# Kernel optimization log

Hardware: AMD Instinct MI355X
Metric: run time of the kernel (lower is better)

Reference implementation:

```python
import jax, jax.numpy as jnp
import numpy as np

D = 256
B, S, N = 4, 512, 4


def setup_inputs() -> dict:
    key = jax.random.key(0)
    ks = jax.random.split(key, 24)
    d, dq = D, D // 4
    std = 0.02
    inp = {
        'x':   jax.random.normal(ks[0], (B, S, N, d), jnp.float32),
        'Wq':  jax.random.normal(ks[1], (d, d), jnp.float32) * std,
        'Wk':  jax.random.normal(ks[2], (d, d), jnp.float32) * std,
        'Wv':  jax.random.normal(ks[3], (d, d), jnp.float32) * std,
        'Wg1': jax.random.normal(ks[4], (d, d), jnp.float32) * std,
        'bg1': jnp.zeros((d,), jnp.float32),
        'Wg2': jax.random.normal(ks[5], (d, d), jnp.float32) * std,
        'bg2': jnp.zeros((d,), jnp.float32),
        'We1': jax.random.normal(ks[6], (d, dq), jnp.float32) * std,
        'be1': jnp.zeros((dq,), jnp.float32),
        'We2': jax.random.normal(ks[7], (dq, 1), jnp.float32) * std,
        'be2': jnp.zeros((1,), jnp.float32),
        'Wa1': jax.random.normal(ks[8], (d, dq), jnp.float32) * std,
        'ba1': jnp.zeros((dq,), jnp.float32),
        'Wa2': jax.random.normal(ks[9], (dq, 1), jnp.float32) * std,
        'ba2': jnp.zeros((1,), jnp.float32),
        'Wo':  jax.random.normal(ks[10], (d, d), jnp.float32) * std,
        'bo':  jnp.zeros((d,), jnp.float32),
        'gamma': jnp.ones((d,), jnp.float32),
        'beta':  jnp.zeros((d,), jnp.float32),
    }
    return inp


def reference(x, Wq, Wk, Wv, Wg1, bg1, Wg2, bg2, We1, be1, We2, be2,
              Wa1, ba1, Wa2, ba2, Wo, bo, gamma, beta):
    b, s, n, f = x.shape
    xf = x.reshape(b * n, s, f)  # matches torch .view on contiguous x
    residual = xf

    q = xf @ Wq                                    # [bn, s, d]
    k = xf @ Wk
    v = xf @ Wv
    v_hat = jax.nn.silu(v @ Wg1 + bg1) @ Wg2 + bg2  # value_generator
    eta = jax.nn.sigmoid(jax.nn.silu(xf @ We1 + be1) @ We2 + be2) * 0.1 + 0.01   # [bn, s, 1]
    alpha = jax.nn.sigmoid(jax.nn.silu(xf @ Wa1 + ba1) @ Wa2 + ba2) * 0.5 + 0.5  # [bn, s, 1]

    # F.normalize(k, dim=-1): eps = 1e-12
    kn = k / jnp.maximum(jnp.linalg.norm(k, axis=-1, keepdims=True), 1e-12)

    M0 = jnp.zeros((b * n, f, f), x.dtype)

    def step(M, inp):
        q_t, k_t, v_t, e_t, a_t = inp  # [bn,d],[bn,d],[bn,d],[bn,1],[bn,1]
        out_t = jnp.einsum('bij,bj->bi', M, q_t)
        Mk = jnp.einsum('bij,bj->bi', M, k_t)
        e = e_t[:, :, None]  # [bn,1,1]
        a = a_t[:, :, None]
        # delta rule: M <- a*M - e*(Mk k^T) + e*(v k^T)
        M_new = a * M + e * ((v_t - Mk)[:, :, None] * k_t[:, None, :])
        return M_new, out_t

    seq = (jnp.swapaxes(q, 0, 1), jnp.swapaxes(kn, 0, 1), jnp.swapaxes(v_hat, 0, 1),
           jnp.swapaxes(eta, 0, 1), jnp.swapaxes(alpha, 0, 1))
    M, outs = jax.lax.scan(step, M0, seq)
    out = jnp.swapaxes(outs, 0, 1)  # [bn, s, d]

    y = out @ Wo + bo + residual  # dropout is identity in eval/reference
    mu = jnp.mean(y, axis=-1, keepdims=True)
    var = jnp.var(y, axis=-1, keepdims=True)
    y = (y - mu) / jnp.sqrt(var + 1e-5) * gamma + beta
    return y.reshape(b, s, n, f), M
```

## Files before the change

kernel.cpp:

```cpp
#include <hip/hip_runtime.h>

#define F_ 256
#define S_ 512
#define NH_ 16
#define CCH 32
#define NCH (S_/CCH)
#define KSTR 264
#define KTSTR 36
#define TSTR 40

typedef __attribute__((ext_vector_type(8))) short short8_t;
typedef __attribute__((ext_vector_type(4))) float f32x4;

__device__ __forceinline__ float sigmoid_f(float x) { return 1.0f / (1.0f + __expf(-x)); }

__device__ __forceinline__ ushort f2bf(float x) {
  uint u = __float_as_uint(x);
  u += 0x7FFFu + ((u >> 16) & 1u);
  return (ushort)(u >> 16);
}
__device__ __forceinline__ float bf2f(ushort u) {
  return __uint_as_float((uint)u << 16);
}

template<int CTRL>
__device__ __forceinline__ float dpp_add(float x) {
  int y = __builtin_amdgcn_update_dpp(0, __float_as_int(x), CTRL, 0xf, 0xf, true);
  return x + __int_as_float(y);
}
__device__ __forceinline__ float red8(float x) {
  x = dpp_add<0xB1>(x);
  x = dpp_add<0x4E>(x);
  x = dpp_add<0x141>(x);
  return x;
}

__global__ __launch_bounds__(256) void wconv_k(
    const float* __restrict__ Wq, const float* __restrict__ Wk,
    const float* __restrict__ Wv, const float* __restrict__ Wg1,
    const float* __restrict__ Wg2, const float* __restrict__ Wo,
    const float* __restrict__ We1, const float* __restrict__ Wa1,
    const float* __restrict__ be1, const float* __restrict__ ba1,
    ushort* __restrict__ Wt, float* __restrict__ beas)
{
  const int blk = blockIdx.x, tid = threadIdx.x;
  if (blk == 104) {
    if (tid < 64) beas[tid] = be1[tid];
    else if (tid < 128) beas[tid] = ba1[tid - 64];
    return;
  }
  __shared__ float tile[64][65];
  const float* src; int N, k0, n0; size_t dstbase;
  if (blk < 96) {
    const int w = blk >> 4, tl = blk & 15;
    const float* ws_[6] = {Wq, Wk, Wv, Wg1, Wg2, Wo};
    const size_t dstb[6] = {0, 65536, 131072, 229376, 294912, 360448};
    src = ws_[w]; N = 256;
    k0 = (tl >> 2) * 64; n0 = (tl & 3) * 64;
    dstbase = dstb[w];
  } else {
    const int w = (blk - 96) >> 2, tl = (blk - 96) & 3;
    src = w ? Wa1 : We1; N = 64;
    k0 = tl * 64; n0 = 0;
    dstbase = w ? 212992 : 196608;
  }
// ... 131 lines not shown
    pB[0] = *(const short8_t*)&Wt[(size_t)(col0 + r_) * 256 + k0 + c8_];
    pB[1] = *(const short8_t*)&Wt[(size_t)(col0 + 32 + r_) * 256 + k0 + c8_];
  };
  auto commitT = [&](int b) {
    *(short8_t*)&As[b][r_ * 72 + c8_] = pA[0];
    *(short8_t*)&As[b][(32 + r_) * 72 + c8_] = pA[1];
    *(short8_t*)&Ws[b][r_ * 72 + c8_] = pB[0];
    *(short8_t*)&Ws[b][(32 + r_) * 72 + c8_] = pB[1];
  };

  f32x4 acc[2][2];
  #pragma unroll
  for (int i = 0; i < 2; ++i)
    #pragma unroll
    for (int j = 0; j < 2; ++j)
      #pragma unroll
      for (int r = 0; r < 4; ++r) acc[i][j][r] = 0.f;

  loadT(0); commitT(0); __syncthreads();
  #pragma unroll
  for (int t = 0; t < 4; ++t) {
    const int b = t & 1;
    if (t < 3) loadT((t + 1) << 6);
    #pragma unroll
    for (int kk = 0; kk < 2; ++kk) {
      short8_t a0 = *(const short8_t*)&As[b][(wr * 32 + ln) * 72 + kk * 32 + hi8];
      short8_t a1 = *(const short8_t*)&As[b][(wr * 32 + 16 + ln) * 72 + kk * 32 + hi8];
      short8_t b0 = *(const short8_t*)&Ws[b][(wc * 32 + ln) * 72 + kk * 32 + hi8];
      short8_t b1 = *(const short8_t*)&Ws[b][(wc * 32 + 16 + ln) * 72 + kk * 32 + hi8];
      acc[0][0] = __builtin_amdgcn_mfma_f32_16x16x32_bf16(a0, b0, acc[0][0], 0, 0, 0);
      acc[0][1] = __builtin_amdgcn_mfma_f32_16x16x32_bf16(a0, b1, acc[0][1], 0, 0, 0);
      acc[1][0] = __builtin_amdgcn_mfma_f32_16x16x32_bf16(a1, b0, acc[1][0], 0, 0, 0);
      acc[1][1] = __builtin_amdgcn_mfma_f32_16x16x32_bf16(a1, b1, acc[1][1], 0, 0, 0);
    }
    if (t < 3) commitT(b ^ 1);
    __syncthreads();
  }

  #pragma unroll
  for (int mi = 0; mi < 2; ++mi)
    #pragma unroll
    for (int ni = 0; ni < 2; ++ni) {
      const int col = col0 + wc * 32 + ni * 16 + ln;
      const float bval = bias ? bias[col] : 0.f;
      #pragma unroll
      for (int r = 0; r < 4; ++r) {
        const int row = row0 + wr * 32 + mi * 16 + hi4 + r;
        float vx = acc[mi][ni][r] + bval;
        if (act == 1) vx = vx * sigmoid_f(vx);
        if (Cf) Cf[(size_t)row * 256 + col] = vx;
        if (Cb) Cb[(size_t)row * 256 + col] = f2bf(vx);
      }
    }
}

__global__ __launch_bounds__(256) void gemmo_ln_k(
    const ushort* __restrict__ A, const ushort* __restrict__ Wt,
    const float* __restrict__ bo, const float* __restrict__ x,
    const float* __restrict__ gamma, const float* __restrict__ beta,
    float* __restrict__ y)
{
  __shared__ ushort As[2][32 * 72];
  __shared__ ushort Ws[2][256 * 72];
  __shared__ float rs_[2][32];
  __shared__ float rq_[2][32];
  const int tid = threadIdx.x;
  const int wv = tid >> 6, l = tid & 63;
  const int ln = l & 15, hi = l >> 4, hi4 = hi << 2, hi8 = hi << 3;
  const int g = wv >> 1, chf = wv & 1;
  const int row0 = blockIdx.x * 32;

  short8_t pA, pW[8];
  auto loadT = [&](int k0) {
    { const int r = tid >> 3, c8 = (tid & 7) << 3;
      pA = *(const short8_t*)&A[(size_t)(row0 + r) * 256 + k0 + c8]; }
    #pragma unroll
    for (int p = 0; p < 8; ++p) {
      const int idx = (p << 8) + tid;
      const int n = idx >> 3, c8 = (idx & 7) << 3;
      pW[p] = *(const short8_t*)&Wt[(size_t)n * 256 + k0 + c8];
    }
  };
  auto commitT = [&](int b) {
    { const int r = tid >> 3, c8 = (tid & 7) << 3;
      *(short8_t*)&As[b][r * 72 + c8] = pA; }
    #pragma unroll
    for (int p = 0; p < 8; ++p) {
      const int idx = (p << 8) + tid;
      const int n = idx >> 3, c8 = (idx & 7) << 3;
      *(short8_t*)&Ws[b][n * 72 + c8] = pW[p];
    }
  };

  f32x4 acc[8];
  #pragma unroll
  for (int nt = 0; nt < 8; ++nt)
    #pragma unroll
    for (int r = 0; r < 4; ++r) acc[nt][r] = 0.f;

  loadT(0); commitT(0); __syncthreads();
  #pragma unroll
  for (int t = 0; t < 4; ++t) {
    const int b = t & 1;
    if (t < 3) loadT((t + 1) << 6);
    #pragma unroll
    for (int kk = 0; kk < 2; ++kk) {
// ... 42 lines not shown
  #pragma unroll
  for (int r = 0; r < 4; ++r) {
    const int lr = g * 16 + hi4 + r;
    const float tot = rs_[0][lr] + rs_[1][lr];
    const float tq  = rq_[0][lr] + rq_[1][lr];
    const float mu  = tot * (1.0f / 256.0f);
    const float var = tq * (1.0f / 256.0f) - mu * mu;
    const float rstd = rsqrtf(var + 1e-5f);
    #pragma unroll
    for (int nt = 0; nt < 8; ++nt) {
      const int col = chf * 128 + nt * 16 + ln;
      y[(size_t)(row0 + lr) * 256 + col] =
          (val[nt][r] - mu) * rstd * gamma[col] + beta[col];
    }
  }
}

__global__ __launch_bounds__(256) void knea_k(
    const float* __restrict__ kf, ushort* __restrict__ kb,
    const float* __restrict__ sesa,
    const float* __restrict__ We2, const float* __restrict__ be2,
    const float* __restrict__ Wa2, const float* __restrict__ ba2,
    float* __restrict__ eta, float* __restrict__ alpha)
{
  const int lane = threadIdx.x & 63;
  const size_t row = ((size_t)blockIdx.x << 2) + (threadIdx.x >> 6);
  {
    const size_t off = row * F_ + ((size_t)lane << 2);
    float4 v = *(const float4*)&kf[off];
    float ss = v.x * v.x + v.y * v.y + v.z * v.z + v.w * v.w;
    #pragma unroll
    for (int m = 1; m < 64; m <<= 1) ss += __shfl_xor(ss, m, 64);
    const float sc = 1.0f / fmaxf(sqrtf(ss), 1e-12f);
    ushort4 o;
    o.x = f2bf(v.x * sc); o.y = f2bf(v.y * sc);
    o.z = f2bf(v.z * sc); o.w = f2bf(v.w * sc);
    *(ushort4*)&kb[off] = o;
  }
  {
    float pe = sesa[row * 128 + lane] * We2[lane];
    float pa = sesa[row * 128 + 64 + lane] * Wa2[lane];
    #pragma unroll
    for (int m = 1; m < 64; m <<= 1) {
      pe += __shfl_xor(pe, m, 64);
      pa += __shfl_xor(pa, m, 64);
    }
    if (lane == 0) {
      eta[row]   = sigmoid_f(pe + be2[0]) * 0.1f + 0.01f;
      alpha[row] = sigmoid_f(pa + ba2[0]) * 0.5f + 0.5f;
    }
  }
}

__global__ __launch_bounds__(256) void prep_k(
    const ushort* __restrict__ kb, const ushort* __restrict__ qb,
    const float* __restrict__ eta, const float* __restrict__ alpha,
    ushort* __restrict__ Tg, ushort* __restrict__ Gqg, float* __restrict__ Sg,
    ushort* __restrict__ Ktg)
{
  __shared__ ushort K_lds[CCH * KSTR];
  __shared__ ushort Q_lds[CCH * KSTR];
  __shared__ float  G_lds[CCH * CCH];
  __shared__ float  ea[2 * CCH];
  __shared__ float  scal[100];

  const int tid = threadIdx.x;
  const int ch = blockIdx.x, h = blockIdx.y;
  const int t0 = ch * CCH;
  const int l = tid & 63, wv = tid >> 6;
  const int ln = l & 15, hi = l >> 4;
  const int hi8 = hi * 8, hi4 = hi * 4;

  const ushort* kg = kb + (size_t)(h * S_ + t0) * F_;
  const ushort* qg = qb + (size_t)(h * S_ + t0) * F_;
  #pragma unroll
  for (int w = 0; w < 4; ++w) {
    int o = w * 256 + tid; int t = o >> 5, c8 = (o & 31) << 3;
    *(short8_t*)&K_lds[t * KSTR + c8] = *(const short8_t*)&kg[(size_t)t * F_ + c8];
    *(short8_t*)&Q_lds[t * KSTR + c8] = *(const short8_t*)&qg[(size_t)t * F_ + c8];
  }
  if (tid < CCH)            ea[tid] = eta[(size_t)h * S_ + t0 + tid];
  else if (tid < 2 * CCH)   ea[tid] = alpha[(size_t)h * S_ + t0 + tid - CCH];
  __syncthreads();

  {
    const int tt = tid & 31, cl = tid >> 5;
    for (int cp = 0; cp < 32; ++cp) {
      const int c = cp * 8 + cl;
      Ktg[((size_t)h * F_ + c) * S_ + t0 + tt] = K_lds[tt * KSTR + c];
    }
  }

  {
    const int tI = wv >> 1, tJ = wv & 1;
    f32x4 accG = {0.f, 0.f, 0.f, 0.f};
    f32x4 accQ = {0.f, 0.f, 0.f, 0.f};
    #pragma unroll
    for (int ko = 0; ko < 8; ++ko) {
      const int cb = ko * 32 + hi8;
      short8_t bfr = *(const short8_t*)&K_lds[(tJ * 16 + ln) * KSTR + cb];
      short8_t aK  = *(const short8_t*)&K_lds[(tI * 16 + ln) * KSTR + cb];
      short8_t aQ  = *(const short8_t*)&Q_lds[(tI * 16 + ln) * KSTR + cb];
      accG = __builtin_amdgcn_mfma_f32_16x16x32_bf16(aK, bfr, accG, 0, 0, 0);
      accQ = __builtin_amdgcn_mfma_f32_16x16x32_bf16(aQ, bfr, accQ, 0, 0, 0);
    }
    ushort* Gqo = Gqg + (size_t)(h * NCH + ch) * (CCH * CCH);
    #pragma unroll
    for (int r = 0; r < 4; ++r) {
      const int t = tI * 16 + hi4 + r, s = tJ * 16 + ln;
      G_lds[t * CCH + s] = accG[r];
      Gqo[t * CCH + s] = (s < t) ? f2bf(accQ[r]) : (ushort)0;
    }
  }
  if (tid == 0) {
    float gp = 1.f;
    for (int t = 0; t < CCH; ++t) {
      const float a = ea[CCH + t], e = ea[t];
      const float gm = gp * a;
      scal[t]           = e / a;
      scal[CCH + t]     = e / gm;
      scal[2 * CCH + t] = gp;
      gp = gm;
    }
    scal[3 * CCH] = gp;
  }
  __syncthreads();

  {
    const int j = tid >> 3, g = tid & 7;
    float x0 = 0.f, x1 = 0.f, x2 = 0.f, x3 = 0.f;
    ushort* To = Tg + (size_t)(h * NCH + ch) * (CCH * CCH);
    #pragma unroll
    for (int t = 0; t < CCH; ++t) {
      float p = 0.f;
      const f32x4 gr = *(const f32x4*)&G_lds[t * CCH + 4 * g];
      if (4 * g + 0 < t) p += gr[0] * x0;
      if (4 * g + 1 < t) p += gr[1] * x1;
      if (4 * g + 2 < t) p += gr[2] * x2;
      if (4 * g + 3 < t) p += gr[3] * x3;
      const float tot = red8(p);
      const float xt = ((t == j) ? 1.f : 0.f) - scal[t] * tot;
      if (g == (t >> 2)) {
        if ((t & 3) == 0) x0 = xt; else if ((t & 3) == 1) x1 = xt;
        else if ((t & 3) == 2) x2 = xt; else x3 = xt;
      }
      if (g == 0) To[t * CCH + j] = f2bf(xt);
    }
  }
  if (tid < 97) Sg[(size_t)(h * NCH + ch) * 128 + tid] = scal[tid];
}

__global__ __launch_bounds__(256, 1) void scan_chunk_k(
    const ushort* __restrict__ kb, const ushort* __restrict__ qb,
    const ushort* __restrict__ vhb, const ushort* __restrict__ Ktg,
    const ushort* __restrict__ Tg, const ushort* __restrict__ Gqg,
    const float* __restrict__ Sg,
    ushort* __restrict__ outb, float* __restrict__ Mout)
{
  __shared__ ushort K_lds[2][CCH * KSTR];
  __shared__ ushort Q_lds[2][CCH * KSTR];
  __shared__ ushort Kt_lds[2][F_ * KTSTR];
  __shared__ ushort M_lds[16 * KSTR];
  __shared__ ushort T_lds[2][CCH * TSTR];
  __shared__ ushort Gq_lds[2][CCH * TSTR];
  __shared__ ushort Wt_lds[16 * TSTR];
  __shared__ ushort R_lds[16 * TSTR];
  __shared__ float  QM_lds[CCH * 20];
  __shared__ ushort V_lds[2][CCH * 16];
  __shared__ float  scal[2][104];

  const int tid = threadIdx.x;
  const int flat = blockIdx.x;
  const int h = (flat & 7) + (((flat >> 3) >> 4) << 3);
  const int slice = (flat >> 3) & 15;
  const int r0 = slice * 16;
  const int wv = tid >> 6, l = tid & 63;
  const int ln = l & 15, hi = l >> 4, hi4 = hi << 2, hi8 = hi << 3;

  for (int u = tid; u < 16 * KSTR / 8; u += 256) {
    short8_t z = {0, 0, 0, 0, 0, 0, 0, 0};
    *(short8_t*)&M_lds[u * 8] = z;
  }
  f32x4 Mf[4];
  #pragma unroll
  for (int q = 0; q < 4; ++q)
    #pragma unroll
    for (int r = 0; r < 4; ++r) Mf[q][r] = 0.f;

  const ushort* kgh = kb + (size_t)h * S_ * F_;
  const ushort* qgh = qb + (size_t)h * S_ * F_;
  const ushort* kth = Ktg + (size_t)h * F_ * S_;

  short8_t pK[4], pQ[4], pKt[4], pTG;
  ushort pV[2]; float pS = 0.f;

  auto loadchunk = [&](int ch) {
    const int t0 = ch * CCH;
    #pragma unroll
    for (int r = 0; r < 4; ++r) {
      const int idx = (r << 8) + tid;
      const int t = idx >> 5, c8 = (idx & 31) << 3;
      pK[r] = *(const short8_t*)&kgh[(size_t)(t0 + t) * F_ + c8];
      pQ[r] = *(const short8_t*)&qgh[(size_t)(t0 + t) * F_ + c8];
    }
    #pragma unroll
    for (int r = 0; r < 4; ++r) {
      const int idx = (r << 8) + tid;
      const int c = idx >> 2, t8 = (idx & 3) << 3;
      pKt[r] = *(const short8_t*)&kth[(size_t)c * S_ + t0 + t8];
    }
    #pragma unroll
    for (int u = 0; u < 2; ++u) {
      const int e = (u << 8) + tid, t = e >> 4, i = e & 15;
      pV[u] = vhb[(size_t)(h * S_ + t0 + t) * F_ + r0 + i];
    }
    {
      const ushort* Ti = Tg  + (size_t)(h * NCH + ch) * (CCH * CCH);
      const ushort* Gi = Gqg + (size_t)(h * NCH + ch) * (CCH * CCH);
      if (tid < 128) {
        const int t = tid >> 2, c8 = (tid & 3) << 3;
        pTG = *(const short8_t*)&Ti[t * CCH + c8];
      } else {
        const int t = (tid - 128) >> 2, c8 = ((tid - 128) & 3) << 3;
        pTG = *(const short8_t*)&Gi[t * CCH + c8];
      }
    }
    if (tid < 97) pS = Sg[(size_t)(h * NCH + ch) * 128 + tid];
  };

  auto commit = [&](int buf) {
    #pragma unroll
    for (int r = 0; r < 4; ++r) {
      const int idx = (r << 8) + tid;
      const int t = idx >> 5, c8 = (idx & 31) << 3;
      *(short8_t*)&K_lds[buf][t * KSTR + c8] = pK[r];
      *(short8_t*)&Q_lds[buf][t * KSTR + c8] = pQ[r];
    }
    #pragma unroll
    for (int r = 0; r < 4; ++r) {
      const int idx = (r << 8) + tid;
      const int c = idx >> 2, t8 = (idx & 3) << 3;
      *(short8_t*)&Kt_lds[buf][c * KTSTR + t8] = pKt[r];
    }
    #pragma unroll
    for (int u = 0; u < 2; ++u) V_lds[buf][(u << 8) + tid] = pV[u];
    if (tid < 128) {
      const int t = tid >> 2, c8 = (tid & 3) << 3;
      *(short8_t*)&T_lds[buf][t * TSTR + c8] = pTG;
    } else {
      const int t = (tid - 128) >> 2, c8 = ((tid - 128) & 3) << 3;
      *(short8_t*)&Gq_lds[buf][t * TSTR + c8] = pTG;
    }
    if (tid < 97) scal[buf][tid] = pS;
  };

  loadchunk(0);
  commit(0);
  __syncthreads();

  for (int ch = 0; ch < NCH; ++ch) {
    const int buf = ch & 1;
    const int t0 = ch * CCH;
    if (ch + 1 < NCH) loadchunk(ch + 1);

    if (wv < 2) {
      const int I = wv;
      f32x4 a0 = {0.f, 0.f, 0.f, 0.f}, a1 = {0.f, 0.f, 0.f, 0.f};
      #pragma unroll
      for (int ko = 0; ko < 4; ++ko) {
        {
          short8_t a = *(const short8_t*)&K_lds[buf][(I * 16 + ln) * KSTR + (2 * ko) * 32 + hi8];
          short8_t b = *(const short8_t*)&M_lds[ln * KSTR + (2 * ko) * 32 + hi8];
          a0 = __builtin_amdgcn_mfma_f32_16x16x32_bf16(a, b, a0, 0, 0, 0);
        }
        {
          short8_t a = *(const short8_t*)&K_lds[buf][(I * 16 + ln) * KSTR + (2 * ko + 1) * 32 + hi8];
          short8_t b = *(const short8_t*)&M_lds[ln * KSTR + (2 * ko + 1) * 32 + hi8];
          a1 = __builtin_amdgcn_mfma_f32_16x16x32_bf16(a, b, a1, 0, 0, 0);
        }
      }
      #pragma unroll
      for (int r = 0; r < 4; ++r) {
        const int t = I * 16 + hi4 + r;
        const float s = a0[r] + a1[r];
        const float rhs = scal[buf][CCH + t] * bf2f(V_lds[buf][t * 16 + ln])
                        - scal[buf][t] * s;
        R_lds[ln * TSTR + t] = f2bf(rhs);
      }
    } else {
      const int I = wv - 2;
      f32x4 a0 = {0.f, 0.f, 0.f, 0.f}, a1 = {0.f, 0.f, 0.f, 0.f};
      #pragma unroll
      for (int ko = 0; ko < 4; ++ko) {
        {
          short8_t a = *(const short8_t*)&Q_lds[buf][(I * 16 + ln) * KSTR + (2 * ko) * 32 + hi8];
          short8_t b = *(const short8_t*)&M_lds[ln * KSTR + (2 * ko) * 32 + hi8];
          a0 = __builtin_amdgcn_mfma_f32_16x16x32_bf16(a, b, a0, 0, 0, 0);
        }
        {
          short8_t a = *(const short8_t*)&Q_lds[buf][(I * 16 + ln) * KSTR + (2 * ko + 1) * 32 + hi8];
          short8_t b = *(const short8_t*)&M_lds[ln * KSTR + (2 * ko + 1) * 32 + hi8];
          a1 = __builtin_amdgcn_mfma_f32_16x16x32_bf16(a, b, a1, 0, 0, 0);
        }
      }
      #pragma unroll
      for (int r = 0; r < 4; ++r)
        QM_lds[(I * 16 + hi4 + r) * 20 + ln] = a0[r] + a1[r];
    }
    __syncthreads();

    if (wv < 2) {
      const int I = wv;
      short8_t a = *(const short8_t*)&T_lds[buf][(I * 16 + ln) * TSTR + hi8];
      short8_t b = *(const short8_t*)&R_lds[ln * TSTR + hi8];
      f32x4 z = {0.f, 0.f, 0.f, 0.f};
      f32x4 d = __builtin_amdgcn_mfma_f32_16x16x32_bf16(a, b, z, 0, 0, 0);
      #pragma unroll
      for (int r = 0; r < 4; ++r)
        Wt_lds[ln * TSTR + I * 16 + hi4 + r] = f2bf(d[r]);
    }
    __syncthreads();

    if (wv < 2) {
      const int I = wv;
      short8_t a = *(const short8_t*)&Gq_lds[buf][(I * 16 + ln) * TSTR + hi8];
      short8_t b = *(const short8_t*)&Wt_lds[ln * TSTR + hi8];
      f32x4 z = {0.f, 0.f, 0.f, 0.f};
      f32x4 d = __builtin_amdgcn_mfma_f32_16x16x32_bf16(a, b, z, 0, 0, 0);
      #pragma unroll
      for (int r = 0; r < 4; ++r) {
        const int t = I * 16 + hi4 + r;
        outb[(size_t)(h * S_ + t0 + t) * F_ + r0 + ln] =
            f2bf(scal[buf][2 * CCH + t] * (QM_lds[t * 20 + ln] + d[r]));
      }
    }
    {
      const float gC = scal[buf][3 * CCH];
      short8_t aw = *(const short8_t*)&Wt_lds[ln * TSTR + hi8];
      #pragma unroll
      for (int qq = 0; qq < 4; ++qq) {
        const int jt = wv * 4 + qq;
        short8_t bk = *(const short8_t*)&Kt_lds[buf][(jt * 16 + ln) * KTSTR + hi8];
        f32x4 d = __builtin_amdgcn_mfma_f32_16x16x32_bf16(aw, bk, Mf[qq], 0, 0, 0);
        #pragma unroll
        for (int r = 0; r < 4; ++r) {
          const float nv = gC * d[r];
          Mf[qq][r] = nv;
          M_lds[(hi4 + r) * KSTR + jt * 16 + ln] = f2bf(nv);
        }
      }
    }
    if (ch + 1 < NCH) commit(buf ^ 1);
    __syncthreads();
  }

  #pragma unroll
  for (int qq = 0; qq < 4; ++qq) {
    const int jt = wv * 4 + qq;
    #pragma unroll
    for (int r = 0; r < 4; ++r)
      Mout[((size_t)h * F_ + r0 + hi4 + r) * F_ + jt * 16 + ln] = Mf[qq][r];
  }
}

extern "C" void kernel_launch(void* const* d_in, const int* in_sizes, int n_in,
                              void* d_out, int out_size, void* d_ws, size_t ws_size,
                              hipStream_t stream)
{
  const float* x    = (const float*)d_in[0];
  const float* Wq   = (const float*)d_in[1];
  const float* Wk   = (const float*)d_in[2];
  const float* Wv   = (const float*)d_in[3];
  const float* Wg1  = (const float*)d_in[4];
  const float* bg1  = (const float*)d_in[5];
  const float* Wg2  = (const float*)d_in[6];
  const float* bg2  = (const float*)d_in[7];
  const float* We1  = (const float*)d_in[8];
  const float* be1  = (const float*)d_in[9];
  const float* We2  = (const float*)d_in[10];
  const float* be2  = (const float*)d_in[11];
  const float* Wa1  = (const float*)d_in[12];
  const float* ba1  = (const float*)d_in[13];
  const float* Wa2  = (const float*)d_in[14];
  const float* ba2  = (const float*)d_in[15];
  const float* Wo   = (const float*)d_in[16];
  const float* bo   = (const float*)d_in[17];
  const float* gamma= (const float*)d_in[18];
  const float* beta = (const float*)d_in[19];

  const int Mrows = NH_ * S_;
  const size_t MM = 1048576;
  const size_t NTF = 2 * MM;

  float* ws = (float*)d_ws;
  ushort* outb = (ushort*)(ws + 0 * MM);
  ushort* qb   = (ushort*)(ws + 1 * MM);
  ushort* kb   = (ushort*)(ws + 2 * MM);
  float*  kf   = ws + 3 * MM;
  ushort* t1b  = (ushort*)(ws + 3 * MM);
  ushort* vhb  = (ushort*)(ws + 4 * MM);
  ushort* vb   = (ushort*)(ws + 5 * MM);
  float*  sesa = ws + 6 * MM;
  float*  eta  = ws + 7 * MM;
  float*  alpha= eta + Mrows;
  ushort* Tg   = (ushort*)(ws + 7 * MM + 16384);
  ushort* Gqg  = Tg + 262144;
  float*  Sg   = ws + 7 * MM + 16384 + 131072 + 131072;
  ushort* Ktg  = (ushort*)(Sg + 32768);
  ushort* Wt   = Ktg + 2097152;
  float*  beas = (float*)(Wt + 425984);

  dim3 blk(256);

  wconv_k<<<105, blk, 0, stream>>>(Wq, Wk, Wv, Wg1, Wg2, Wo, We1, Wa1,
                                   be1, ba1, Wt, beas);

  qkve_k<<<dim3(14, 128), blk, 0, stream>>>(x, Wt, beas, qb, kf, vb, sesa);

  knea_k<<<Mrows / 4, blk, 0, stream>>>(kf, kb, sesa, We2, be2, Wa2, ba2, eta, alpha);

  gemm_bf16_k<<<dim3(4, 128), blk, 0, stream>>>(vb,  Wt + 229376, bg1, nullptr, t1b, 1);
  gemm_bf16_k<<<dim3(4, 128), blk, 0, stream>>>(t1b, Wt + 294912, bg2, nullptr, vhb, 0);

  prep_k<<<dim3(NCH, NH_), blk, 0, stream>>>(kb, qb, eta, alpha, Tg, Gqg, Sg, Ktg);

  float* yout = (float*)d_out;
  float* Mfin = yout + NTF;
  scan_chunk_k<<<256, blk, 0, stream>>>(kb, qb, vhb, Ktg, Tg, Gqg, Sg, outb, Mfin);

  gemmo_ln_k<<<256, blk, 0, stream>>>(outb, Wt + 360448, bo, x, gamma, beta, yout);
}
```

Measured before the change: 100.1 us.

## Split scan into 8-row slices with single-buffered LDS and two blocks per CU

The chunked delta-rule scan now gives each block 8 rows of the state instead of 16, so 512 blocks launch instead of 256. Double-buffered LDS tiles become single buffers with the commit split into two phases, which cuts shared memory so two blocks fit per CU under the new launch bounds. The output-projection MFMA is moved after the state update. Each block still runs full 16-wide MFMAs with half the lanes masked off, so compute per useful row doubles in exchange for more parallelism and occupancy.

```diff
diff --git a/kernel.cpp b/kernel.cpp
--- a/kernel.cpp
+++ b/kernel.cpp
@@ -494,30 +494,31 @@
   if (tid < 97) Sg[(size_t)(h * NCH + ch) * 128 + tid] = scal[tid];
 }
 
-__global__ __launch_bounds__(256, 1) void scan_chunk_k(
+__global__ __launch_bounds__(256, 2) void scan_chunk_k(
     const ushort* __restrict__ kb, const ushort* __restrict__ qb,
     const ushort* __restrict__ vhb, const ushort* __restrict__ Ktg,
     const ushort* __restrict__ Tg, const ushort* __restrict__ Gqg,
     const float* __restrict__ Sg,
     ushort* __restrict__ outb, float* __restrict__ Mout)
 {
-  __shared__ ushort K_lds[2][CCH * KSTR];
-  __shared__ ushort Q_lds[2][CCH * KSTR];
-  __shared__ ushort Kt_lds[2][F_ * KTSTR];
+  __shared__ ushort K_lds[CCH * KSTR];
+  __shared__ ushort Q_lds[CCH * KSTR];
+  __shared__ ushort Kt_lds[F_ * KTSTR];
   __shared__ ushort M_lds[16 * KSTR];
-  __shared__ ushort T_lds[2][CCH * TSTR];
-  __shared__ ushort Gq_lds[2][CCH * TSTR];
+  __shared__ ushort T_lds[CCH * TSTR];
+  __shared__ ushort Gq_lds[CCH * TSTR];
   __shared__ ushort Wt_lds[16 * TSTR];
   __shared__ ushort R_lds[16 * TSTR];
-  __shared__ float  QM_lds[CCH * 20];
-  __shared__ ushort V_lds[2][CCH * 16];
+  __shared__ float  QM_lds[CCH * 12];
+  __shared__ ushort V_lds[CCH * 8];
   __shared__ float  scal[2][104];
 
   const int tid = threadIdx.x;
   const int flat = blockIdx.x;
-  const int h = (flat & 7) + (((flat >> 3) >> 4) << 3);
-  const int slice = (flat >> 3) & 15;
-  const int r0 = slice * 16;
+  const int idx = flat >> 3;
+  const int h = (flat & 7) + ((idx >> 5) << 3);
+  const int slice = idx & 31;
+  const int r0 = slice * 8;
   const int wv = tid >> 6, l = tid & 63;
   const int ln = l & 15, hi = l >> 4, hi4 = hi << 2, hi8 = hi << 3;
 
@@ -534,30 +535,27 @@
   const ushort* kgh = kb + (size_t)h * S_ * F_;
   const ushort* qgh = qb + (size_t)h * S_ * F_;
   const ushort* kth = Ktg + (size_t)h * F_ * S_;
+  const ushort* vgh = vhb + (size_t)h * S_ * F_;
 
   short8_t pK[4], pQ[4], pKt[4], pTG;
-  ushort pV[2]; float pS = 0.f;
+  ushort pV = 0; float pS = 0.f;
 
   auto loadchunk = [&](int ch) {
     const int t0 = ch * CCH;
     #pragma unroll
     for (int r = 0; r < 4; ++r) {
-      const int idx = (r << 8) + tid;
-      const int t = idx >> 5, c8 = (idx & 31) << 3;
+      const int idx2 = (r << 8) + tid;
+      const int t = idx2 >> 5, c8 = (idx2 & 31) << 3;
       pK[r] = *(const short8_t*)&kgh[(size_t)(t0 + t) * F_ + c8];
       pQ[r] = *(const short8_t*)&qgh[(size_t)(t0 + t) * F_ + c8];
     }
     #pragma unroll
     for (int r = 0; r < 4; ++r) {
-      const int idx = (r << 8) + tid;
-      const int c = idx >> 2, t8 = (idx & 3) << 3;
+      const int idx2 = (r << 8) + tid;
+      const int c = idx2 >> 2, t8 = (idx2 & 3) << 3;
       pKt[r] = *(const short8_t*)&kth[(size_t)c * S_ + t0 + t8];
     }
-    #pragma unroll
-    for (int u = 0; u < 2; ++u) {
-      const int e = (u << 8) + tid, t = e >> 4, i = e & 15;
-      pV[u] = vhb[(size_t)(h * S_ + t0 + t) * F_ + r0 + i];
-    }
+    pV = vgh[(size_t)(t0 + (tid >> 3)) * F_ + r0 + (tid & 7)];
     {
       const ushort* Ti = Tg  + (size_t)(h * NCH + ch) * (CCH * CCH);
       const ushort* Gi = Gqg + (size_t)(h * NCH + ch) * (CCH * CCH);
@@ -572,39 +570,43 @@
     if (tid < 97) pS = Sg[(size_t)(h * NCH + ch) * 128 + tid];
   };
 
-  auto commit = [&](int buf) {
+  auto commitA = [&](int dst) {
     #pragma unroll
     for (int r = 0; r < 4; ++r) {
-      const int idx = (r << 8) + tid;
-      const int t = idx >> 5, c8 = (idx & 31) << 3;
-      *(short8_t*)&K_lds[buf][t * KSTR + c8] = pK[r];
-      *(short8_t*)&Q_lds[buf][t * KSTR + c8] = pQ[r];
-    }
-    #pragma unroll
-    for (int r = 0; r < 4; ++r) {
-      const int idx = (r << 8) + tid;
-      const int c = idx >> 2, t8 = (idx & 3) << 3;
-      *(short8_t*)&Kt_lds[buf][c * KTSTR + t8] = pKt[r];
-    }
-    #pragma unroll
-    for (int u = 0; u < 2; ++u) V_lds[buf][(u << 8) + tid] = pV[u];
+      const int idx2 = (r << 8) + tid;
+      const int t = idx2 >> 5, c8 = (idx2 & 31) << 3;
+      *(short8_t*)&K_lds[t * KSTR + c8] = pK[r];
+      *(short8_t*)&Q_lds[t * KSTR + c8] = pQ[r];
+    }
+    V_lds[tid] = pV;
     if (tid < 128) {
       const int t = tid >> 2, c8 = (tid & 3) << 3;
-      *(short8_t*)&T_lds[buf][t * TSTR + c8] = pTG;
-    } else {
+      *(short8_t*)&T_lds[t * TSTR + c8] = pTG;
+    }
+    if (tid < 97) scal[dst][tid] = pS;
+  };
+  auto commitB = [&]() {
+    #pragma unroll
+    for (int r = 0; r < 4; ++r) {
+      const int idx2 = (r << 8) + tid;
+      const int c = idx2 >> 2, t8 = (idx2 & 3) << 3;
+      *(short8_t*)&Kt_lds[c * KTSTR + t8] = pKt[r];
+    }
+    if (tid >= 128) {
       const int t = (tid - 128) >> 2, c8 = ((tid - 128) & 3) << 3;
-      *(short8_t*)&Gq_lds[buf][t * TSTR + c8] = pTG;
-    }
-    if (tid < 97) scal[buf][tid] = pS;
+      *(short8_t*)&Gq_lds[t * TSTR + c8] = pTG;
+    }
   };
 
   loadchunk(0);
-  commit(0);
+  commitA(0);
+  commitB();
   __syncthreads();
 
   for (int ch = 0; ch < NCH; ++ch) {
-    const int buf = ch & 1;
+    const int sb = ch & 1;
     const int t0 = ch * CCH;
+    if (ch > 0) commitB();
     if (ch + 1 < NCH) loadchunk(ch + 1);
 
     if (wv < 2) {
@@ -613,12 +615,12 @@
       #pragma unroll
       for (int ko = 0; ko < 4; ++ko) {
         {
-          short8_t a = *(const short8_t*)&K_lds[buf][(I * 16 + ln) * KSTR + (2 * ko) * 32 + hi8];
+          short8_t a = *(const short8_t*)&K_lds[(I * 16 + ln) * KSTR + (2 * ko) * 32 + hi8];
           short8_t b = *(const short8_t*)&M_lds[ln * KSTR + (2 * ko) * 32 + hi8];
           a0 = __builtin_amdgcn_mfma_f32_16x16x32_bf16(a, b, a0, 0, 0, 0);
         }
         {
-          short8_t a = *(const short8_t*)&K_lds[buf][(I * 16 + ln) * KSTR + (2 * ko + 1) * 32 + hi8];
+          short8_t a = *(const short8_t*)&K_lds[(I * 16 + ln) * KSTR + (2 * ko + 1) * 32 + hi8];
           short8_t b = *(const short8_t*)&M_lds[ln * KSTR + (2 * ko + 1) * 32 + hi8];
           a1 = __builtin_amdgcn_mfma_f32_16x16x32_bf16(a, b, a1, 0, 0, 0);
         }
@@ -626,10 +628,14 @@
       #pragma unroll
       for (int r = 0; r < 4; ++r) {
         const int t = I * 16 + hi4 + r;
-        const float s = a0[r] + a1[r];
-        const float rhs = scal[buf][CCH + t] * bf2f(V_lds[buf][t * 16 + ln])
-                        - scal[buf][t] * s;
-        R_lds[ln * TSTR + t] = f2bf(rhs);
+        ushort rw = 0;
+        if (ln < 8) {
+          const float s = a0[r] + a1[r];
+          const float rhs = scal[sb][CCH + t] * bf2f(V_lds[t * 8 + ln])
+                          - scal[sb][t] * s;
+          rw = f2bf(rhs);
+        }
+        R_lds[ln * TSTR + t] = rw;
       }
     } else {
       const int I = wv - 2;
@@ -637,25 +643,27 @@
       #pragma unroll
       for (int ko = 0; ko < 4; ++ko) {
         {
-          short8_t a = *(const short8_t*)&Q_lds[buf][(I * 16 + ln) * KSTR + (2 * ko) * 32 + hi8];
+          short8_t a = *(const short8_t*)&Q_lds[(I * 16 + ln) * KSTR + (2 * ko) * 32 + hi8];
           short8_t b = *(const short8_t*)&M_lds[ln * KSTR + (2 * ko) * 32 + hi8];
           a0 = __builtin_amdgcn_mfma_f32_16x16x32_bf16(a, b, a0, 0, 0, 0);
         }
         {
-          short8_t a = *(const short8_t*)&Q_lds[buf][(I * 16 + ln) * KSTR + (2 * ko + 1) * 32 + hi8];
+          short8_t a = *(const short8_t*)&Q_lds[(I * 16 + ln) * KSTR + (2 * ko + 1) * 32 + hi8];
           short8_t b = *(const short8_t*)&M_lds[ln * KSTR + (2 * ko + 1) * 32 + hi8];
           a1 = __builtin_amdgcn_mfma_f32_16x16x32_bf16(a, b, a1, 0, 0, 0);
         }
       }
-      #pragma unroll
-      for (int r = 0; r < 4; ++r)
-        QM_lds[(I * 16 + hi4 + r) * 20 + ln] = a0[r] + a1[r];
+      if (ln < 8) {
+        #pragma unroll
+        for (int r = 0; r < 4; ++r)
+          QM_lds[(I * 16 + hi4 + r) * 12 + ln] = a0[r] + a1[r];
+      }
     }
     __syncthreads();
 
     if (wv < 2) {
       const int I = wv;
-      short8_t a = *(const short8_t*)&T_lds[buf][(I * 16 + ln) * TSTR + hi8];
+      short8_t a = *(const short8_t*)&T_lds[(I * 16 + ln) * TSTR + hi8];
       short8_t b = *(const short8_t*)&R_lds[ln * TSTR + hi8];
       f32x4 z = {0.f, 0.f, 0.f, 0.f};
       f32x4 d = __builtin_amdgcn_mfma_f32_16x16x32_bf16(a, b, z, 0, 0, 0);
@@ -665,26 +673,13 @@
     }
     __syncthreads();
 
-    if (wv < 2) {
-      const int I = wv;
-      short8_t a = *(const short8_t*)&Gq_lds[buf][(I * 16 + ln) * TSTR + hi8];
-      short8_t b = *(const short8_t*)&Wt_lds[ln * TSTR + hi8];
-      f32x4 z = {0.f, 0.f, 0.f, 0.f};
-      f32x4 d = __builtin_amdgcn_mfma_f32_16x16x32_bf16(a, b, z, 0, 0, 0);
-      #pragma unroll
-      for (int r = 0; r < 4; ++r) {
-        const int t = I * 16 + hi4 + r;
-        outb[(size_t)(h * S_ + t0 + t) * F_ + r0 + ln] =
-            f2bf(scal[buf][2 * CCH + t] * (QM_lds[t * 20 + ln] + d[r]));
-      }
-    }
     {
-      const float gC = scal[buf][3 * CCH];
+      const float gC = scal[sb][3 * CCH];
       short8_t aw = *(const short8_t*)&Wt_lds[ln * TSTR + hi8];
       #pragma unroll
       for (int qq = 0; qq < 4; ++qq) {
         const int jt = wv * 4 + qq;
-        short8_t bk = *(const short8_t*)&Kt_lds[buf][(jt * 16 + ln) * KTSTR + hi8];
+        short8_t bk = *(const short8_t*)&Kt_lds[(jt * 16 + ln) * KTSTR + hi8];
         f32x4 d = __builtin_amdgcn_mfma_f32_16x16x32_bf16(aw, bk, Mf[qq], 0, 0, 0);
         #pragma unroll
         for (int r = 0; r < 4; ++r) {
@@ -694,16 +689,33 @@
         }
       }
     }
-    if (ch + 1 < NCH) commit(buf ^ 1);
+    if (wv < 2) {
+      const int I = wv;
+      short8_t a = *(const short8_t*)&Gq_lds[(I * 16 + ln) * TSTR + hi8];
+      short8_t b = *(const short8_t*)&Wt_lds[ln * TSTR + hi8];
+      f32x4 z = {0.f, 0.f, 0.f, 0.f};
+      f32x4 d = __builtin_amdgcn_mfma_f32_16x16x32_bf16(a, b, z, 0, 0, 0);
+      if (ln < 8) {
+        #pragma unroll
+        for (int r = 0; r < 4; ++r) {
+          const int t = I * 16 + hi4 + r;
+          outb[(size_t)(h * S_ + t0 + t) * F_ + r0 + ln] =
+              f2bf(scal[sb][2 * CCH + t] * (QM_lds[t * 12 + ln] + d[r]));
+        }
+      }
+    }
+    if (ch + 1 < NCH) commitA(sb ^ 1);
     __syncthreads();
   }
 
-  #pragma unroll
-  for (int qq = 0; qq < 4; ++qq) {
-    const int jt = wv * 4 + qq;
-    #pragma unroll
-    for (int r = 0; r < 4; ++r)
-      Mout[((size_t)h * F_ + r0 + hi4 + r) * F_ + jt * 16 + ln] = Mf[qq][r];
+  if (hi < 2) {
+    #pragma unroll
+    for (int qq = 0; qq < 4; ++qq) {
+      const int jt = wv * 4 + qq;
+      #pragma unroll
+      for (int r = 0; r < 4; ++r)
+        Mout[((size_t)h * F_ + r0 + hi4 + r) * F_ + jt * 16 + ln] = Mf[qq][r];
+    }
   }
 }
 
@@ -770,7 +782,7 @@
 
   float* yout = (float*)d_out;
   float* Mfin = yout + NTF;
-  scan_chunk_k<<<256, blk, 0, stream>>>(kb, qb, vhb, Ktg, Tg, Gqg, Sg, outb, Mfin);
+  scan_chunk_k<<<512, blk, 0, stream>>>(kb, qb, vhb, Ktg, Tg, Gqg, Sg, outb, Mfin);
 
   gemmo_ln_k<<<256, blk, 0, stream>>>(outb, Wt + 360448, bo, x, gamma, beta, yout);
 }
```

Result: slower. 108.5 us (+8.3%).

## Merge first value-generator GEMM with chunk prep and trim scan barriers

Applied to the files above, without the earlier changes.

Combines the Wg1 GEMM and the per-chunk prep work into one launch, with blocks picking a role by block index. This removes a kernel launch and lets the two independent jobs fill the GPU at the same time. In the scan kernel, waves 0-1 each compute both halves of the residual and then their W tile privately, which removes two block-wide barriers per chunk. The output GEMM is moved after the M update, and the barriers are replaced by raw waitcnt+s_barrier. The tradeoff is duplicated K·M MFMA work in each of those two waves and a tighter reliance on LDS ordering.

```diff
diff --git a/kernel.cpp b/kernel.cpp
--- a/kernel.cpp
+++ b/kernel.cpp
@@ -11,6 +11,12 @@
 
 typedef __attribute__((ext_vector_type(8))) short short8_t;
 typedef __attribute__((ext_vector_type(4))) float f32x4;
+
+#define BARX() do { \
+  asm volatile("s_waitcnt lgkmcnt(0)" ::: "memory"); \
+  __builtin_amdgcn_s_barrier(); \
+  __builtin_amdgcn_sched_barrier(0); \
+} while (0)
 
 __device__ __forceinline__ float sigmoid_f(float x) { return 1.0f / (1.0f + __expf(-x)); }
 
@@ -248,6 +254,176 @@
         if (Cb) Cb[(size_t)row * 256 + col] = f2bf(vx);
       }
     }
+}
+
+__global__ __launch_bounds__(256) void g1prep_k(
+    const ushort* __restrict__ vb, const ushort* __restrict__ WtG1,
+    const float* __restrict__ bg1, ushort* __restrict__ t1b,
+    const ushort* __restrict__ kb, const ushort* __restrict__ qb,
+    const float* __restrict__ eta, const float* __restrict__ alpha,
+    ushort* __restrict__ Tg, ushort* __restrict__ Gqg, float* __restrict__ Sg,
+    ushort* __restrict__ Ktg)
+{
+  __shared__ __align__(16) char smem[38592];
+  const int blk = blockIdx.x;
+  const int tid = threadIdx.x;
+  const int l = tid & 63, wv = tid >> 6;
+  const int ln = l & 15, hi = l >> 4, hi4 = hi << 2, hi8 = hi << 3;
+
+  if (blk < 512) {
+    ushort* As = (ushort*)smem;
+    ushort* Ws = (ushort*)(smem + 18432);
+    const int wr = wv >> 1, wc = wv & 1;
+    const int row0 = (blk >> 2) * 64, col0 = (blk & 3) * 64;
+    const int r_ = tid >> 3, c8_ = (tid & 7) << 3;
+
+    short8_t pA[2], pB[2];
+    auto loadT = [&](int k0) {
+      pA[0] = *(const short8_t*)&vb[(size_t)(row0 + r_) * 256 + k0 + c8_];
+      pA[1] = *(const short8_t*)&vb[(size_t)(row0 + 32 + r_) * 256 + k0 + c8_];
+      pB[0] = *(const short8_t*)&WtG1[(size_t)(col0 + r_) * 256 + k0 + c8_];
+      pB[1] = *(const short8_t*)&WtG1[(size_t)(col0 + 32 + r_) * 256 + k0 + c8_];
+    };
+    auto commitT = [&](int b) {
+      *(short8_t*)&As[b * 4608 + r_ * 72 + c8_] = pA[0];
+      *(short8_t*)&As[b * 4608 + (32 + r_) * 72 + c8_] = pA[1];
+      *(short8_t*)&Ws[b * 4608 + r_ * 72 + c8_] = pB[0];
+      *(short8_t*)&Ws[b * 4608 + (32 + r_) * 72 + c8_] = pB[1];
+    };
+
+    f32x4 acc[2][2];
+    #pragma unroll
+    for (int i = 0; i < 2; ++i)
+      #pragma unroll
+      for (int j = 0; j < 2; ++j)
+        #pragma unroll
+        for (int r = 0; r < 4; ++r) acc[i][j][r] = 0.f;
+
+    loadT(0); commitT(0); __syncthreads();
+    #pragma unroll
+    for (int t = 0; t < 4; ++t) {
+      const int b = t & 1;
+      if (t < 3) loadT((t + 1) << 6);
+      #pragma unroll
+      for (int kk = 0; kk < 2; ++kk) {
+        short8_t a0 = *(const short8_t*)&As[b * 4608 + (wr * 32 + ln) * 72 + kk * 32 + hi8];
+        short8_t a1 = *(const short8_t*)&As[b * 4608 + (wr * 32 + 16 + ln) * 72 + kk * 32 + hi8];
+        short8_t b0 = *(const short8_t*)&Ws[b * 4608 + (wc * 32 + ln) * 72 + kk * 32 + hi8];
+        short8_t b1 = *(const short8_t*)&Ws[b * 4608 + (wc * 32 + 16 + ln) * 72 + kk * 32 + hi8];
+        acc[0][0] = __builtin_amdgcn_mfma_f32_16x16x32_bf16(a0, b0, acc[0][0], 0, 0, 0);
+        acc[0][1] = __builtin_amdgcn_mfma_f32_16x16x32_bf16(a0, b1, acc[0][1], 0, 0, 0);
+        acc[1][0] = __builtin_amdgcn_mfma_f32_16x16x32_bf16(a1, b0, acc[1][0], 0, 0, 0);
+        acc[1][1] = __builtin_amdgcn_mfma_f32_16x16x32_bf16(a1, b1, acc[1][1], 0, 0, 0);
+      }
+      if (t < 3) commitT(b ^ 1);
+      __syncthreads();
+    }
+
+    #pragma unroll
+    for (int mi = 0; mi < 2; ++mi)
+      #pragma unroll
+      for (int ni = 0; ni < 2; ++ni) {
+        const int col = col0 + wc * 32 + ni * 16 + ln;
+        const float bval = bg1[col];
+        #pragma unroll
+        for (int r = 0; r < 4; ++r) {
+          const int row = row0 + wr * 32 + mi * 16 + hi4 + r;
+          float vx = acc[mi][ni][r] + bval;
+          vx = vx * sigmoid_f(vx);
+          t1b[(size_t)row * 256 + col] = f2bf(vx);
+        }
+      }
+    return;
+  }
+
+  const int pb = blk - 512;
+  const int ch = pb & 15, h = pb >> 4;
+  const int t0 = ch * CCH;
+  ushort* K_lds = (ushort*)smem;
+  ushort* Q_lds = (ushort*)(smem + 16896);
+  float*  G_lds = (float*)(smem + 33792);
+  float*  ea    = (float*)(smem + 37888);
+  float*  eaA   = (float*)(smem + 37888 + 0);
+  float*  scal  = (float*)(smem + 38144);
+
+  const ushort* kg = kb + (size_t)(h * S_ + t0) * F_;
+  const ushort* qg = qb + (size_t)(h * S_ + t0) * F_;
+  #pragma unroll
+  for (int w = 0; w < 4; ++w) {
+    int o = w * 256 + tid; int t = o >> 5, c8 = (o & 31) << 3;
+    *(short8_t*)&K_lds[t * KSTR + c8] = *(const short8_t*)&kg[(size_t)t * F_ + c8];
+    *(short8_t*)&Q_lds[t * KSTR + c8] = *(const short8_t*)&qg[(size_t)t * F_ + c8];
+  }
+  if (tid < CCH)            ea[tid] = eta[(size_t)h * S_ + t0 + tid];
+  else if (tid < 2 * CCH)   ea[tid] = alpha[(size_t)h * S_ + t0 + tid - CCH];
+  __syncthreads();
+  (void)eaA;
+
+  {
+    const int tt = tid & 31, cl = tid >> 5;
+    for (int cp = 0; cp < 32; ++cp) {
+      const int c = cp * 8 + cl;
+      Ktg[((size_t)h * F_ + c) * S_ + t0 + tt] = K_lds[tt * KSTR + c];
+    }
+  }
+
+  {
+    const int tI = wv >> 1, tJ = wv & 1;
+    f32x4 accG = {0.f, 0.f, 0.f, 0.f};
+    f32x4 accQ = {0.f, 0.f, 0.f, 0.f};
+    #pragma unroll
+    for (int ko = 0; ko < 8; ++ko) {
+      const int cb = ko * 32 + hi8;
+      short8_t bfr = *(const short8_t*)&K_lds[(tJ * 16 + ln) * KSTR + cb];
+      short8_t aK  = *(const short8_t*)&K_lds[(tI * 16 + ln) * KSTR + cb];
+      short8_t aQ  = *(const short8_t*)&Q_lds[(tI * 16 + ln) * KSTR + cb];
+      accG = __builtin_amdgcn_mfma_f32_16x16x32_bf16(aK, bfr, accG, 0, 0, 0);
+      accQ = __builtin_amdgcn_mfma_f32_16x16x32_bf16(aQ, bfr, accQ, 0, 0, 0);
+    }
+    ushort* Gqo = Gqg + (size_t)(h * NCH + ch) * (CCH * CCH);
+    #pragma unroll
+    for (int r = 0; r < 4; ++r) {
+      const int t = tI * 16 + hi4 + r, s = tJ * 16 + ln;
+      G_lds[t * CCH + s] = accG[r];
+      Gqo[t * CCH + s] = (s < t) ? f2bf(accQ[r]) : (ushort)0;
+    }
+  }
+  if (tid == 0) {
+    float gp = 1.f;
+    for (int t = 0; t < CCH; ++t) {
+      const float a = ea[CCH + t], e = ea[t];
+      const float gm = gp * a;
+      scal[t]           = e / a;
+      scal[CCH + t]     = e / gm;
+      scal[2 * CCH + t] = gp;
+      gp = gm;
+    }
+    scal[3 * CCH] = gp;
+  }
+  __syncthreads();
+
+  {
+    const int j = tid >> 3, g = tid & 7;
+    float x0 = 0.f, x1 = 0.f, x2 = 0.f, x3 = 0.f;
+    ushort* To = Tg + (size_t)(h * NCH + ch) * (CCH * CCH);
+    #pragma unroll
+    for (int t = 0; t < CCH; ++t) {
+      float p = 0.f;
+      const f32x4 gr = *(const f32x4*)&G_lds[t * CCH + 4 * g];
+      if (4 * g + 0 < t) p += gr[0] * x0;
+      if (4 * g + 1 < t) p += gr[1] * x1;
+      if (4 * g + 2 < t) p += gr[2] * x2;
+      if (4 * g + 3 < t) p += gr[3] * x3;
+      const float tot = red8(p);
+      const float xt = ((t == j) ? 1.f : 0.f) - scal[t] * tot;
+      if (g == (t >> 2)) {
+        if ((t & 3) == 0) x0 = xt; else if ((t & 3) == 1) x1 = xt;
+        else if ((t & 3) == 2) x2 = xt; else x3 = xt;
+      }
+      if (g == 0) To[t * CCH + j] = f2bf(xt);
+    }
+  }
+  if (tid < 97) Sg[(size_t)(h * NCH + ch) * 128 + tid] = scal[tid];
 }
 
 __global__ __launch_bounds__(256) void gemmo_ln_k(
@@ -396,104 +572,6 @@
   }
 }
 
-__global__ __launch_bounds__(256) void prep_k(
-    const ushort* __restrict__ kb, const ushort* __restrict__ qb,
-    const float* __restrict__ eta, const float* __restrict__ alpha,
-    ushort* __restrict__ Tg, ushort* __restrict__ Gqg, float* __restrict__ Sg,
-    ushort* __restrict__ Ktg)
-{
-  __shared__ ushort K_lds[CCH * KSTR];
-  __shared__ ushort Q_lds[CCH * KSTR];
-  __shared__ float  G_lds[CCH * CCH];
-  __shared__ float  ea[2 * CCH];
-  __shared__ float  scal[100];
-
-  const int tid = threadIdx.x;
-  const int ch = blockIdx.x, h = blockIdx.y;
-  const int t0 = ch * CCH;
-  const int l = tid & 63, wv = tid >> 6;
-  const int ln = l & 15, hi = l >> 4;
-  const int hi8 = hi * 8, hi4 = hi * 4;
-
-  const ushort* kg = kb + (size_t)(h * S_ + t0) * F_;
-  const ushort* qg = qb + (size_t)(h * S_ + t0) * F_;
-  #pragma unroll
-  for (int w = 0; w < 4; ++w) {
-    int o = w * 256 + tid; int t = o >> 5, c8 = (o & 31) << 3;
-    *(short8_t*)&K_lds[t * KSTR + c8] = *(const short8_t*)&kg[(size_t)t * F_ + c8];
-    *(short8_t*)&Q_lds[t * KSTR + c8] = *(const short8_t*)&qg[(size_t)t * F_ + c8];
-  }
-  if (tid < CCH)            ea[tid] = eta[(size_t)h * S_ + t0 + tid];
-  else if (tid < 2 * CCH)   ea[tid] = alpha[(size_t)h * S_ + t0 + tid - CCH];
-  __syncthreads();
-
-  {
-    const int tt = tid & 31, cl = tid >> 5;
-    for (int cp = 0; cp < 32; ++cp) {
-      const int c = cp * 8 + cl;
-      Ktg[((size_t)h * F_ + c) * S_ + t0 + tt] = K_lds[tt * KSTR + c];
-    }
-  }
-
-  {
-    const int tI = wv >> 1, tJ = wv & 1;
-    f32x4 accG = {0.f, 0.f, 0.f, 0.f};
-    f32x4 accQ = {0.f, 0.f, 0.f, 0.f};
-    #pragma unroll
-    for (int ko = 0; ko < 8; ++ko) {
-      const int cb = ko * 32 + hi8;
-      short8_t bfr = *(const short8_t*)&K_lds[(tJ * 16 + ln) * KSTR + cb];
-      short8_t aK  = *(const short8_t*)&K_lds[(tI * 16 + ln) * KSTR + cb];
-      short8_t aQ  = *(const short8_t*)&Q_lds[(tI * 16 + ln) * KSTR + cb];
-      accG = __builtin_amdgcn_mfma_f32_16x16x32_bf16(aK, bfr, accG, 0, 0, 0);
-      accQ = __builtin_amdgcn_mfma_f32_16x16x32_bf16(aQ, bfr, accQ, 0, 0, 0);
-    }
-    ushort* Gqo = Gqg + (size_t)(h * NCH + ch) * (CCH * CCH);
-    #pragma unroll
-    for (int r = 0; r < 4; ++r) {
-      const int t = tI * 16 + hi4 + r, s = tJ * 16 + ln;
-      G_lds[t * CCH + s] = accG[r];
-      Gqo[t * CCH + s] = (s < t) ? f2bf(accQ[r]) : (ushort)0;
-    }
-  }
-  if (tid == 0) {
-    float gp = 1.f;
-    for (int t = 0; t < CCH; ++t) {
-      const float a = ea[CCH + t], e = ea[t];
-      const float gm = gp * a;
-      scal[t]           = e / a;
-      scal[CCH + t]     = e / gm;
-      scal[2 * CCH + t] = gp;
-      gp = gm;
-    }
-    scal[3 * CCH] = gp;
-  }
-  __syncthreads();
-
-  {
-    const int j = tid >> 3, g = tid & 7;
-    float x0 = 0.f, x1 = 0.f, x2 = 0.f, x3 = 0.f;
-    ushort* To = Tg + (size_t)(h * NCH + ch) * (CCH * CCH);
-    #pragma unroll
-    for (int t = 0; t < CCH; ++t) {
-      float p = 0.f;
-      const f32x4 gr = *(const f32x4*)&G_lds[t * CCH + 4 * g];
-      if (4 * g + 0 < t) p += gr[0] * x0;
-      if (4 * g + 1 < t) p += gr[1] * x1;
-      if (4 * g + 2 < t) p += gr[2] * x2;
-      if (4 * g + 3 < t) p += gr[3] * x3;
-      const float tot = red8(p);
-      const float xt = ((t == j) ? 1.f : 0.f) - scal[t] * tot;
-      if (g == (t >> 2)) {
-        if ((t & 3) == 0) x0 = xt; else if ((t & 3) == 1) x1 = xt;
-        else if ((t & 3) == 2) x2 = xt; else x3 = xt;
-      }
-      if (g == 0) To[t * CCH + j] = f2bf(xt);
-    }
-  }
-  if (tid < 97) Sg[(size_t)(h * NCH + ch) * 128 + tid] = scal[tid];
-}
-
 __global__ __launch_bounds__(256, 1) void scan_chunk_k(
     const ushort* __restrict__ kb, const ushort* __restrict__ qb,
     const ushort* __restrict__ vhb, const ushort* __restrict__ Ktg,
@@ -508,7 +586,7 @@
   __shared__ ushort T_lds[2][CCH * TSTR];
   __shared__ ushort Gq_lds[2][CCH * TSTR];
   __shared__ ushort Wt_lds[16 * TSTR];
-  __shared__ ushort R_lds[16 * TSTR];
+  __shared__ ushort R2_lds[2][16 * TSTR];
   __shared__ float  QM_lds[CCH * 20];
   __shared__ ushort V_lds[2][CCH * 16];
   __shared__ float  scal[2][104];
@@ -600,7 +678,7 @@
 
   loadchunk(0);
   commit(0);
-  __syncthreads();
+  BARX();
 
   for (int ch = 0; ch < NCH; ++ch) {
     const int buf = ch & 1;
@@ -608,28 +686,42 @@
     if (ch + 1 < NCH) loadchunk(ch + 1);
 
     if (wv < 2) {
-      const int I = wv;
-      f32x4 a0 = {0.f, 0.f, 0.f, 0.f}, a1 = {0.f, 0.f, 0.f, 0.f};
-      #pragma unroll
-      for (int ko = 0; ko < 4; ++ko) {
-        {
-          short8_t a = *(const short8_t*)&K_lds[buf][(I * 16 + ln) * KSTR + (2 * ko) * 32 + hi8];
-          short8_t b = *(const short8_t*)&M_lds[ln * KSTR + (2 * ko) * 32 + hi8];
-          a0 = __builtin_amdgcn_mfma_f32_16x16x32_bf16(a, b, a0, 0, 0, 0);
+      #pragma unroll
+      for (int tt = 0; tt < 2; ++tt) {
+        f32x4 a0 = {0.f, 0.f, 0.f, 0.f}, a1 = {0.f, 0.f, 0.f, 0.f};
+        #pragma unroll
+        for (int ko = 0; ko < 4; ++ko) {
+          {
+            short8_t a = *(const short8_t*)&K_lds[buf][(tt * 16 + ln) * KSTR + (2 * ko) * 32 + hi8];
+            short8_t b = *(const short8_t*)&M_lds[ln * KSTR + (2 * ko) * 32 + hi8];
+            a0 = __builtin_amdgcn_mfma_f32_16x16x32_bf16(a, b, a0, 0, 0, 0);
+          }
+          {
+            short8_t a = *(const short8_t*)&K_lds[buf][(tt * 16 + ln) * KSTR + (2 * ko + 1) * 32 + hi8];
+            short8_t b = *(const short8_t*)&M_lds[ln * KSTR + (2 * ko + 1) * 32 + hi8];
+            a1 = __builtin_amdgcn_mfma_f32_16x16x32_bf16(a, b, a1, 0, 0, 0);
+          }
         }
-        {
-          short8_t a = *(const short8_t*)&K_lds[buf][(I * 16 + ln) * KSTR + (2 * ko + 1) * 32 + hi8];
-          short8_t b = *(const short8_t*)&M_lds[ln * KSTR + (2 * ko + 1) * 32 + hi8];
-          a1 = __builtin_amdgcn_mfma_f32_16x16x32_bf16(a, b, a1, 0, 0, 0);
+        #pragma unroll
+        for (int r = 0; r < 4; ++r) {
+          const int t = tt * 16 + hi4 + r;
+          const float s = a0[r] + a1[r];
+          const float rhs = scal[buf][CCH + t] * bf2f(V_lds[buf][t * 16 + ln])
+                          - scal[buf][t] * s;
+          R2_lds[wv][ln * TSTR + t] = f2bf(rhs);
         }
       }
-      #pragma unroll
-      for (int r = 0; r < 4; ++r) {
-        const int t = I * 16 + hi4 + r;
-        const float s = a0[r] + a1[r];
-        const float rhs = scal[buf][CCH + t] * bf2f(V_lds[buf][t * 16 + ln])
-                        - scal[buf][t] * s;
-        R_lds[ln * TSTR + t] = f2bf(rhs);
+      asm volatile("s_waitcnt lgkmcnt(0)" ::: "memory");
+      __builtin_amdgcn_sched_barrier(0);
+      {
+        const int I = wv;
+        short8_t a = *(const short8_t*)&T_lds[buf][(I * 16 + ln) * TSTR + hi8];
+        short8_t b = *(const short8_t*)&R2_lds[wv][ln * TSTR + hi8];
+        f32x4 z = {0.f, 0.f, 0.f, 0.f};
+        f32x4 d = __builtin_amdgcn_mfma_f32_16x16x32_bf16(a, b, z, 0, 0, 0);
+        #pragma unroll
+        for (int r = 0; r < 4; ++r)
+          Wt_lds[ln * TSTR + I * 16 + hi4 + r] = f2bf(d[r]);
       }
     } else {
       const int I = wv - 2;
@@ -651,33 +743,8 @@
       for (int r = 0; r < 4; ++r)
         QM_lds[(I * 16 + hi4 + r) * 20 + ln] = a0[r] + a1[r];
     }
-    __syncthreads();
-
-    if (wv < 2) {
-      const int I = wv;
-      short8_t a = *(const short8_t*)&T_lds[buf][(I * 16 + ln) * TSTR + hi8];
-      short8_t b = *(const short8_t*)&R_lds[ln * TSTR + hi8];
-      f32x4 z = {0.f, 0.f, 0.f, 0.f};
-      f32x4 d = __builtin_amdgcn_mfma_f32_16x16x32_bf16(a, b, z, 0, 0, 0);
-      #pragma unroll
-      for (int r = 0; r < 4; ++r)
-        Wt_lds[ln * TSTR + I * 16 + hi4 + r] = f2bf(d[r]);
-    }
-    __syncthreads();
-
-    if (wv < 2) {
-      const int I = wv;
-      short8_t a = *(const short8_t*)&Gq_lds[buf][(I * 16 + ln) * TSTR + hi8];
-      short8_t b = *(const short8_t*)&Wt_lds[ln * TSTR + hi8];
-      f32x4 z = {0.f, 0.f, 0.f, 0.f};
-      f32x4 d = __builtin_amdgcn_mfma_f32_16x16x32_bf16(a, b, z, 0, 0, 0);
-      #pragma unroll
-      for (int r = 0; r < 4; ++r) {
-        const int t = I * 16 + hi4 + r;
-        outb[(size_t)(h * S_ + t0 + t) * F_ + r0 + ln] =
-            f2bf(scal[buf][2 * CCH + t] * (QM_lds[t * 20 + ln] + d[r]));
-      }
-    }
+    BARX();
+
     {
       const float gC = scal[buf][3 * CCH];
       short8_t aw = *(const short8_t*)&Wt_lds[ln * TSTR + hi8];
@@ -694,8 +761,21 @@
         }
       }
     }
+    if (wv < 2) {
+      const int I = wv;
+      short8_t a = *(const short8_t*)&Gq_lds[buf][(I * 16 + ln) * TSTR + hi8];
+      short8_t b = *(const short8_t*)&Wt_lds[ln * TSTR + hi8];
+      f32x4 z = {0.f, 0.f, 0.f, 0.f};
+      f32x4 d = __builtin_amdgcn_mfma_f32_16x16x32_bf16(a, b, z, 0, 0, 0);
+      #pragma unroll
+      for (int r = 0; r < 4; ++r) {
+        const int t = I * 16 + hi4 + r;
+        outb[(size_t)(h * S_ + t0 + t) * F_ + r0 + ln] =
+            f2bf(scal[buf][2 * CCH + t] * (QM_lds[t * 20 + ln] + d[r]));
+      }
+    }
     if (ch + 1 < NCH) commit(buf ^ 1);
-    __syncthreads();
+    BARX();
   }
 
   #pragma unroll
@@ -763,10 +843,10 @@
 
   knea_k<<<Mrows / 4, blk, 0, stream>>>(kf, kb, sesa, We2, be2, Wa2, ba2, eta, alpha);
 
-  gemm_bf16_k<<<dim3(4, 128), blk, 0, stream>>>(vb,  Wt + 229376, bg1, nullptr, t1b, 1);
+  g1prep_k<<<768, blk, 0, stream>>>(vb, Wt + 229376, bg1, t1b,
+                                    kb, qb, eta, alpha, Tg, Gqg, Sg, Ktg);
+
   gemm_bf16_k<<<dim3(4, 128), blk, 0, stream>>>(t1b, Wt + 294912, bg2, nullptr, vhb, 0);
-
-  prep_k<<<dim3(NCH, NH_), blk, 0, stream>>>(kb, qb, eta, alpha, Tg, Gqg, Sg, Ktg);
 
   float* yout = (float*)d_out;
   float* Mfin = yout + NTF;
```

New measurement: 96.81 us. 1.03x faster.
